# Optimization experiments

Measured on AMD Instinct MI355X. Metric: run time of the kernel, lower is better.

Reference implementation:

```python
import jax, jax.numpy as jnp
import numpy as np

B, S, DM = 1, 4096, 2048
H, HD = 16, 128
TS = 16          # tile_size
TOPK = 16        # anchor tiles per query
NUM_TILES = S // TS


def setup_inputs() -> dict:
    key = jax.random.key(0)
    ks = jax.random.split(key, 7)
    x = jax.random.normal(ks[0], (B, S, DM), jnp.float32)
    Wq = jax.random.normal(ks[1], (DM, H * HD), jnp.float32) * 0.02
    Wk = jax.random.normal(ks[2], (DM, H * HD), jnp.float32) * 0.02
    Wv = jax.random.normal(ks[3], (DM, H * HD), jnp.float32) * 0.02
    Wo = jax.random.normal(ks[4], (H * HD, DM), jnp.float32) * 0.02
    # RoPE angles: pos * inv_freq, shape [S, HD//2] (= freqs_cis angle)
    inv_freq = 1.0 / (10000.0 ** (np.arange(0, HD, 2, dtype=np.float32) / HD))
    freqs = jnp.asarray(np.arange(S, dtype=np.float32)[:, None] * inv_freq[None, :])
    anchor_indices = jax.random.randint(ks[5], (B, H, S, TOPK), 0, NUM_TILES).astype(jnp.int32)
    return {"x": x, "Wq": Wq, "Wk": Wk, "Wv": Wv, "Wo": Wo,
            "freqs": freqs, "anchor_indices": anchor_indices}


def _rotate_half(z):
    half = z.shape[-1] // 2
    return jnp.concatenate([-z[..., half:], z[..., :half]], axis=-1)


def reference(x, Wq, Wk, Wv, Wo, freqs, anchor_indices):
    b, s, _ = x.shape
    num_tiles = s // TS
    # QKV projections -> [B, H, S, HD]
    q = (x @ Wq).reshape(b, s, H, HD).transpose(0, 2, 1, 3)
    k = (x @ Wk).reshape(b, s, H, HD).transpose(0, 2, 1, 3)
    v = (x @ Wv).reshape(b, s, H, HD).transpose(0, 2, 1, 3)
    # RoPE (half-split / rotate_half convention), float32
    cos = jnp.cos(freqs)[None, None, :s, :]
    sin = jnp.sin(freqs)[None, None, :s, :]
    cos_full = jnp.concatenate([cos, cos], axis=-1)
    sin_full = jnp.concatenate([sin, sin], axis=-1)
    q = q * cos_full + _rotate_half(q) * sin_full
    k = k * cos_full + _rotate_half(k) * sin_full
    # Per-query tile indices: anchor tiles + local tile
    local_tiles = (jnp.arange(s) // TS).astype(jnp.int32)
    local = jnp.broadcast_to(local_tiles[None, None, :, None], (b, H, s, 1))
    tiles = jnp.concatenate([anchor_indices, local], axis=-1)  # [B,H,S,K+1]
    # Representative query per tile (last token of each query tile)
    tile_repr = jnp.arange(TS - 1, s, TS)
    tile_sel = tiles[:, :, tile_repr, :]                        # [B,H,T,K+1]
    # Expand tile indices to token indices
    offsets = jnp.arange(TS)
    token_idx = tile_sel[..., None] * TS + offsets              # [B,H,T,K+1,TS]
    sparse_len = tile_sel.shape[-1] * TS
    flat_idx = jnp.clip(token_idx.reshape(b, H, num_tiles, sparse_len), 0, s - 1)
    # Gather sparse K/V per (batch, head, query-tile)
    k_flat = k.reshape(b * H, s, HD)
    v_flat = v.reshape(b * H, s, HD)
    idx_flat = flat_idx.reshape(b * H, num_tiles, sparse_len)
    k_sparse = jax.vmap(lambda kv, idx: kv[idx])(k_flat, idx_flat)
    v_sparse = jax.vmap(lambda kv, idx: kv[idx])(v_flat, idx_flat)
    k_sparse = k_sparse.reshape(b, H, num_tiles, sparse_len, HD)
    v_sparse = v_sparse.reshape(b, H, num_tiles, sparse_len, HD)
    # Block-sparse attention per tile
    q_tiled = q.reshape(b, H, num_tiles, TS, HD)
    logits = jnp.einsum('bhtqd,bhtkd->bhtqk', q_tiled, k_sparse) / jnp.sqrt(HD)
    q_pos = jnp.arange(s).reshape(num_tiles, TS)
    future_mask = flat_idx[:, :, :, None, :] > q_pos[None, None, :, :, None]
    logits = jnp.where(future_mask, -1e10, logits)
    weights = jax.nn.softmax(logits, axis=-1)
    all_masked = jnp.all(future_mask, axis=-1, keepdims=True)
    weights = jnp.where(all_masked, 0.0, weights)
    weights = jnp.where(jnp.isnan(weights), 0.0, weights)
    out = jnp.einsum('bhtqk,bhtkd->bhtqd', weights, v_sparse)
    out = out.reshape(b, H, s, HD).transpose(0, 2, 1, 3).reshape(b, s, H * HD)
    return out @ Wo
```

## Files before the change

### kernel.cpp

```cpp
#include <hip/hip_runtime.h>

typedef unsigned short u16;
typedef unsigned int u32;
typedef __attribute__((ext_vector_type(8))) short bf16x8;
typedef __attribute__((ext_vector_type(4))) float f32x4;

__device__ __forceinline__ u16 f2bf(float f) {
  union { float f; u32 u; } v; v.f = f;
  u32 u = v.u;
  return (u16)((u + 0x7FFFu + ((u >> 16) & 1u)) >> 16);
}
__device__ __forceinline__ float bf2f(u16 s) {
  union { u32 u; float f; } v; v.u = ((u32)s) << 16;
  return v.f;
}

__device__ __forceinline__ void async16(const void* g, void* l) {
  __builtin_amdgcn_global_load_lds(
      (__attribute__((address_space(1))) void*)g,
      (__attribute__((address_space(3))) void*)l, 16, 0, 0);
}

__global__ void cast4_kernel(const float* __restrict__ in, u16* __restrict__ out, int n4) {
  int i = blockIdx.x * 256 + threadIdx.x;
  if (i < n4) {
    float4 v = ((const float4*)in)[i];
    ushort4 o;
    o.x = f2bf(v.x); o.y = f2bf(v.y); o.z = f2bf(v.z); o.w = f2bf(v.w);
    ((ushort4*)out)[i] = o;
  }
}

__global__ void transpose_cast_kernel(const float* __restrict__ in, u16* __restrict__ out,
                                      int R, int C) {
  __shared__ float tile[32][33];
  int c0 = blockIdx.x * 32, r0 = blockIdx.y * 32;
  int tx = threadIdx.x, ty = threadIdx.y;
#pragma unroll
  for (int i = ty; i < 32; i += 8) tile[i][tx] = in[(size_t)(r0 + i) * C + c0 + tx];
  __syncthreads();
#pragma unroll
  for (int i = ty; i < 32; i += 8)
    out[(size_t)(c0 + i) * R + r0 + tx] = f2bf(tile[tx][i]);
}

__global__ void trig_kernel(const float* __restrict__ freqs, float* __restrict__ ct,
                            float* __restrict__ st, int n) {
  int i = blockIdx.x * 256 + threadIdx.x;
  if (i < n) { float f = freqs[i]; ct[i] = cosf(f); st[i] = sinf(f); }
}

__global__ void rope_kernel(u16* __restrict__ q, u16* __restrict__ k,
                            const float* __restrict__ ct, const float* __restrict__ st) {
  int i = blockIdx.x * 256 + threadIdx.x;
  int dp = (i & 31) * 2;
  int hh = (i >> 5) & 15;
  int s  = i >> 9;
  float c0 = ct[s * 64 + dp], c1 = ct[s * 64 + dp + 1];
  float s0 = st[s * 64 + dp], s1 = st[s * 64 + dp + 1];
  size_t base = (size_t)s * 2048 + hh * 128 + dp;
  {
    u32 lo = *(u32*)(q + base);
    u32 hi = *(u32*)(q + base + 64);
    float a0 = bf2f((u16)lo), a1 = bf2f((u16)(lo >> 16));
    float b0 = bf2f((u16)hi), b1 = bf2f((u16)(hi >> 16));
    u32 nlo = (u32)f2bf(a0 * c0 - b0 * s0) | ((u32)f2bf(a1 * c1 - b1 * s1) << 16);
    u32 nhi = (u32)f2bf(b0 * c0 + a0 * s0) | ((u32)f2bf(b1 * c1 + a1 * s1) << 16);
    *(u32*)(q + base) = nlo;
    *(u32*)(q + base + 64) = nhi;
  }
  {
    u32 lo = *(u32*)(k + base);
    u32 hi = *(u32*)(k + base + 64);
    float a0 = bf2f((u16)lo), a1 = bf2f((u16)(lo >> 16));
    float b0 = bf2f((u16)hi), b1 = bf2f((u16)(hi >> 16));
    u32 nlo = (u32)f2bf(a0 * c0 - b0 * s0) | ((u32)f2bf(a1 * c1 - b1 * s1) << 16);
    u32 nhi = (u32)f2bf(b0 * c0 + a0 * s0) | ((u32)f2bf(b1 * c1 + a1 * s1) << 16);
    *(u32*)(k + base) = nlo;
    *(u32*)(k + base + 64) = nhi;
  }
}

__global__ void repack_k_kernel(const u16* __restrict__ Kin, u16* __restrict__ Kp) {
  const int h = blockIdx.y;
  const int s0 = blockIdx.x * 64;
  const int tid = threadIdx.x;
#pragma unroll
  for (int i = 0; i < 16; ++i) {
    int idx = i * 256 + tid;
    int r = idx >> 6;
    int d2 = idx & 63;
    u32 kv = ((const u32*)Kin)[(size_t)(s0 + r) * 1024 + h * 64 + d2];
    ((u32*)Kp)[((size_t)h * 4096 + s0 + r) * 64 + d2] = kv;
  }
}

__global__ void repack_v_kernel(const u16* __restrict__ Vin, u16* __restrict__ VT2) {
  const int h = blockIdx.y;
  const int s0 = blockIdx.x * 64;
  const int tid = threadIdx.x;
  __shared__ u16 lv[64][132];
#pragma unroll
  for (int i = 0; i < 16; ++i) {
    int idx = i * 256 + tid;
    int r = idx >> 6;
    int d2 = idx & 63;
    u32 vv = ((const u32*)Vin)[(size_t)(s0 + r) * 1024 + h * 64 + d2];
    *(u32*)(&lv[r][d2 * 2]) = vv;
  }
  __syncthreads();
#pragma unroll
  for (int i = 0; i < 16; ++i) {
    int idx = i * 256 + tid;
    int k2 = idx & 7;
    int d  = (idx >> 3) & 127;
    int tl = idx >> 10;
    u32 lo = lv[tl * 16 + k2 * 2][d];
    u32 hi = lv[tl * 16 + k2 * 2 + 1][d];
    ((u32*)VT2)[(((size_t)h * 256 + blockIdx.x * 4 + tl) * 128 + d) * 8 + k2] = lo | (hi << 16);
  }
}

template <int OUTBF>
__launch_bounds__(256, 2)
__global__ void gemm128_kernel(const u16* __restrict__ A, const u16* __restrict__ Bt,
                               void* __restrict__ C, int M, int N, int K) {
  __shared__ __align__(16) u16 As[128 * 64];
  __shared__ __align__(16) u16 Bs[128 * 64];
  const int tid  = threadIdx.x;
  const int lane = tid & 63;
  const int wave = tid >> 6;
  const int wr = wave >> 1, wc = wave & 1;
  const int brow = blockIdx.y * 128;
  const int bcol = blockIdx.x * 128;

  int a_goff[4], b_goff[4], l_off[4];
#pragma unroll
  for (int i = 0; i < 4; ++i) {
    int p = (wave * 4 + i) * 1024 + lane * 16;
    int row = p >> 7;
    int colb = (p & 127) ^ ((row & 7) << 4);
    a_goff[i] = (brow + row) * K + (colb >> 1);
    b_goff[i] = (bcol + row) * K + (colb >> 1);
    l_off[i] = p;
  }

  f32x4 acc[4][4];
#pragma unroll
  for (int m = 0; m < 4; ++m)
#pragma unroll
    for (int n = 0; n < 4; ++n) acc[m][n] = (f32x4){0.f, 0.f, 0.f, 0.f};

  for (int k0 = 0; k0 < K; k0 += 64) {
#pragma unroll
    for (int i = 0; i < 4; ++i) {
      async16(A + a_goff[i] + k0, (char*)As + l_off[i]);
      async16(Bt + b_goff[i] + k0, (char*)Bs + l_off[i]);
    }
    __syncthreads();
#pragma unroll
    for (int kk = 0; kk < 2; ++kk) {
      bf16x8 af[4], bfr[4];
#pragma unroll
      for (int m = 0; m < 4; ++m) {
        int row = wr * 64 + m * 16 + (lane & 15);
        int byte = (row << 7) + ((kk * 64 + ((lane >> 4) << 4)) ^ ((row & 7) << 4));
        af[m] = *(const bf16x8*)((const char*)As + byte);
      }
#pragma unroll
      for (int n = 0; n < 4; ++n) {
        int row = wc * 64 + n * 16 + (lane & 15);
        int byte = (row << 7) + ((kk * 64 + ((lane >> 4) << 4)) ^ ((row & 7) << 4));
        bfr[n] = *(const bf16x8*)((const char*)Bs + byte);
      }
#pragma unroll
      for (int m = 0; m < 4; ++m)
#pragma unroll
        for (int n = 0; n < 4; ++n)
          acc[m][n] = __builtin_amdgcn_mfma_f32_16x16x32_bf16(af[m], bfr[n], acc[m][n], 0, 0, 0);
    }
    __syncthreads();
  }

  const int r0 = brow + wr * 64;
  const int c0 = bcol + wc * 64;
#pragma unroll
  for (int m = 0; m < 4; ++m)
#pragma unroll
    for (int n = 0; n < 4; ++n)
#pragma unroll
      for (int r = 0; r < 4; ++r) {
        int rr = r0 + m * 16 + ((lane >> 4) << 2) + r;
        int cc = c0 + n * 16 + (lane & 15);
        if (OUTBF) ((u16*)C)[(size_t)rr * N + cc] = f2bf(acc[m][n][r]);
        else       ((float*)C)[(size_t)rr * N + cc] = acc[m][n][r];
      }
}

__launch_bounds__(256, 3)
__global__ void attn_kernel(const u16* __restrict__ Q, const u16* __restrict__ Kp,
                            const u16* __restrict__ VT2, const int* __restrict__ anchors,
                            u16* __restrict__ Out) {
  const int t = blockIdx.x;
  const int h = blockIdx.y;
  __shared__ int tiles[18];
  __shared__ float lg[16][292];
  __shared__ __align__(16) u16 w_lds[16][296];
  const int tid  = threadIdx.x;
  const int lane = tid & 63;
  const int wave = tid >> 6;
  const int g = lane >> 4;
  const int c = lane & 15;

  if (tid < 16) tiles[tid] = anchors[(size_t)((h << 12) + (t * 16 + 15)) * 16 + tid];
  if (tid == 16) tiles[16] = t;
  if (tid == 17) tiles[17] = 0;
  __syncthreads();

  {
    const u16* qbase = Q + (size_t)(t * 16 + c) * 2048 + h * 128 + g * 8;
    bf16x8 qf[4];
#pragma unroll
    for (int ks = 0; ks < 4; ++ks) qf[ks] = *(const bf16x8*)(qbase + ks * 32);
    for (int j = wave; j < 17; j += 4) {
      int tok = tiles[j] * 16 + c;
      const u16* kbase = Kp + ((size_t)h * 4096 + tok) * 128 + g * 8;
      f32x4 a = (f32x4){0.f, 0.f, 0.f, 0.f};
#pragma unroll
      for (int ks = 0; ks < 4; ++ks) {
        bf16x8 kf = *(const bf16x8*)(kbase + ks * 32);
        a = __builtin_amdgcn_mfma_f32_16x16x32_bf16(qf[ks], kf, a, 0, 0, 0);
      }
#pragma unroll
      for (int r = 0; r < 4; ++r) {
        int qrow = g * 4 + r;
        float vv = a[r] * 0.088388347648318447f;
        if (tok > t * 16 + qrow) vv = -1e10f;
        lg[qrow][j * 16 + c] = vv;
      }
    }
  }
  __syncthreads();

  {
    const int r = tid >> 4, cc = tid & 15;
    float vals[17];
    float mx = -3.0e38f;
#pragma unroll
    for (int i = 0; i < 17; ++i) { vals[i] = lg[r][i * 16 + cc]; mx = fmaxf(mx, vals[i]); }
#pragma unroll
    for (int d = 1; d < 16; d <<= 1) mx = fmaxf(mx, __shfl_xor(mx, d, 64));
    float sum = 0.f;
#pragma unroll
    for (int i = 0; i < 17; ++i) { vals[i] = __expf(vals[i] - mx); sum += vals[i]; }
#pragma unroll
    for (int d = 1; d < 16; d <<= 1) sum += __shfl_xor(sum, d, 64);
    float inv = sum > 0.f ? 1.0f / sum : 0.f;
#pragma unroll
    for (int i = 0; i < 17; ++i) w_lds[r][i * 16 + cc] = f2bf(vals[i] * inv);
    w_lds[r][272 + cc] = 0;
  }
  __syncthreads();

  {
    f32x4 o0 = (f32x4){0.f, 0.f, 0.f, 0.f}, o1 = o0;
    const int d0 = wave * 32;
    const size_t hb = (size_t)h * 256;
    const int keyin = (g & 1) * 8;
#pragma unroll
    for (int ks = 0; ks < 9; ++ks) {
      bf16x8 af = *(const bf16x8*)(&w_lds[c][ks * 32 + g * 8]);
      int jt = 2 * ks + (g >> 1);
      const u16* vb = VT2 + (hb + tiles[jt]) * 128 * 16;
      bf16x8 b0 = *(const bf16x8*)(vb + (d0 + c) * 16 + keyin);
      bf16x8 b1 = *(const bf16x8*)(vb + (d0 + 16 + c) * 16 + keyin);
      o0 = __builtin_amdgcn_mfma_f32_16x16x32_bf16(af, b0, o0, 0, 0, 0);
      o1 = __builtin_amdgcn_mfma_f32_16x16x32_bf16(af, b1, o1, 0, 0, 0);
    }
#pragma unroll
    for (int r = 0; r < 4; ++r) {
      int qrow = g * 4 + r;
      size_t base = (size_t)(t * 16 + qrow) * 2048 + h * 128;
      Out[base + d0 + c]      = f2bf(o0[r]);
      Out[base + d0 + 16 + c] = f2bf(o1[r]);
    }
  }
}

extern "C" void kernel_launch(void* const* d_in, const int* in_sizes, int n_in,
                              void* d_out, int out_size, void* d_ws, size_t ws_size,
                              hipStream_t stream) {
  (void)in_sizes; (void)n_in; (void)out_size; (void)ws_size;
  const float* x      = (const float*)d_in[0];
  const float* Wq     = (const float*)d_in[1];
  const float* Wk     = (const float*)d_in[2];
  const float* Wv     = (const float*)d_in[3];
  const float* Wo     = (const float*)d_in[4];
  const float* Wo_f   = (const float*)d_in[4];
  const float* freqs  = (const float*)d_in[5];
  const int* anchors  = (const int*)d_in[6];
  (void)Wo_f;
  float* out = (float*)d_out;

  char* ws = (char*)d_ws;
  const size_t MB = 1024 * 1024;
  u16* xbf   = (u16*)(ws + 0);
  u16* wqT   = (u16*)(ws + 16 * MB);
  u16* wkT   = (u16*)(ws + 24 * MB);
  u16* wvT   = (u16*)(ws + 32 * MB);
  u16* woT   = (u16*)(ws + 40 * MB);
  u16* qbf   = (u16*)(ws + 48 * MB);
  u16* kbf   = (u16*)(ws + 64 * MB);
  u16* vbf   = (u16*)(ws + 80 * MB);
  u16* attnb = (u16*)(ws + 0);
  u16* Kp    = (u16*)(ws + 16 * MB);
  float* ct  = (float*)(ws + 32 * MB);
  float* st  = (float*)(ws + 33 * MB);
  u16* VT2   = (u16*)(ws + 64 * MB);

  cast4_kernel<<<8192, 256, 0, stream>>>(x, xbf, 2097152);
  dim3 tb(32, 8), tg(64, 64);
  transpose_cast_kernel<<<tg, tb, 0, stream>>>(Wq, wqT, 2048, 2048);
  transpose_cast_kernel<<<tg, tb, 0, stream>>>(Wk, wkT, 2048, 2048);
  transpose_cast_kernel<<<tg, tb, 0, stream>>>(Wv, wvT, 2048, 2048);
  transpose_cast_kernel<<<tg, tb, 0, stream>>>(Wo, woT, 2048, 2048);

  dim3 gg(16, 32);
  gemm128_kernel<1><<<gg, 256, 0, stream>>>(xbf, wqT, qbf, 4096, 2048, 2048);
  gemm128_kernel<1><<<gg, 256, 0, stream>>>(xbf, wkT, kbf, 4096, 2048, 2048);
  gemm128_kernel<1><<<gg, 256, 0, stream>>>(xbf, wvT, vbf, 4096, 2048, 2048);
  trig_kernel<<<1024, 256, 0, stream>>>(freqs, ct, st, 262144);
  rope_kernel<<<8192, 256, 0, stream>>>(qbf, kbf, ct, st);
  repack_k_kernel<<<dim3(64, 16), 256, 0, stream>>>(kbf, Kp);
  repack_v_kernel<<<dim3(64, 16), 256, 0, stream>>>(vbf, VT2);
  attn_kernel<<<dim3(256, 16), 256, 0, stream>>>(qbf, Kp, VT2, anchors, attnb);
  gemm128_kernel<0><<<gg, 256, 0, stream>>>(attnb, woT, out, 4096, 2048, 2048);
}
```

Measured before the change: 280.7 us.

## Pipeline GEMMs with triple-buffered LDS and fuse K repack into RoPE

Replaces the 128x128 single-buffered GEMM with a 128x256-tile, 512-thread kernel. The new kernel triple-buffers LDS with async global-to-LDS loads, waits on vmcnt instead of a full barrier per tile, raises wave priority around the MFMA block and swizzles block order for L2 locality. Separately, RoPE now writes rotated K straight into the per-head packed layout, which drops the repack_k kernel and a pass over K. The attention kernel's occupancy hint goes from 3 to 5 blocks per CU, which may force register spills. The larger LDS footprint (about 144KB per block) limits GEMM occupancy.

Measured after the change: 309.7 us. 1.1x slower.

```diff
diff --git a/kernel.cpp b/kernel.cpp
--- a/kernel.cpp
+++ b/kernel.cpp
@@ -50,7 +50,8 @@
   if (i < n) { float f = freqs[i]; ct[i] = cosf(f); st[i] = sinf(f); }
 }
 
-__global__ void rope_kernel(u16* __restrict__ q, u16* __restrict__ k,
+__global__ void rope_kernel(u16* __restrict__ q, const u16* __restrict__ k,
+                            u16* __restrict__ Kp,
                             const float* __restrict__ ct, const float* __restrict__ st) {
   int i = blockIdx.x * 256 + threadIdx.x;
   int dp = (i & 31) * 2;
@@ -70,28 +71,15 @@
     *(u32*)(q + base + 64) = nhi;
   }
   {
-    u32 lo = *(u32*)(k + base);
-    u32 hi = *(u32*)(k + base + 64);
+    u32 lo = *(const u32*)(k + base);
+    u32 hi = *(const u32*)(k + base + 64);
     float a0 = bf2f((u16)lo), a1 = bf2f((u16)(lo >> 16));
     float b0 = bf2f((u16)hi), b1 = bf2f((u16)(hi >> 16));
     u32 nlo = (u32)f2bf(a0 * c0 - b0 * s0) | ((u32)f2bf(a1 * c1 - b1 * s1) << 16);
     u32 nhi = (u32)f2bf(b0 * c0 + a0 * s0) | ((u32)f2bf(b1 * c1 + a1 * s1) << 16);
-    *(u32*)(k + base) = nlo;
-    *(u32*)(k + base + 64) = nhi;
-  }
-}
-
-__global__ void repack_k_kernel(const u16* __restrict__ Kin, u16* __restrict__ Kp) {
-  const int h = blockIdx.y;
-  const int s0 = blockIdx.x * 64;
-  const int tid = threadIdx.x;
-#pragma unroll
-  for (int i = 0; i < 16; ++i) {
-    int idx = i * 256 + tid;
-    int r = idx >> 6;
-    int d2 = idx & 63;
-    u32 kv = ((const u32*)Kin)[(size_t)(s0 + r) * 1024 + h * 64 + d2];
-    ((u32*)Kp)[((size_t)h * 4096 + s0 + r) * 64 + d2] = kv;
+    size_t kpb = ((size_t)hh * 4096 + s) * 128 + dp;
+    *(u32*)(Kp + kpb) = nlo;
+    *(u32*)(Kp + kpb + 64) = nhi;
   }
 }
 
@@ -121,28 +109,73 @@
   }
 }
 
+__device__ __forceinline__ void tile_compute(const char* Asb, const char* Bsb,
+                                             int wm, int wn, int c, int g,
+                                             f32x4 (&acc)[4][4]) {
+  bf16x8 af[2][4], bb[2][4];
+  const int sw = (c & 7) << 4;
+#pragma unroll
+  for (int m = 0; m < 4; ++m) {
+    const int rb = (wm * 64 + m * 16 + c) << 7;
+#pragma unroll
+    for (int ks = 0; ks < 2; ++ks)
+      af[ks][m] = *(const bf16x8*)(Asb + rb + ((((ks * 4 + g) << 4) ^ sw)));
+  }
+#pragma unroll
+  for (int n = 0; n < 4; ++n) {
+    const int rb = (wn * 64 + n * 16 + c) << 7;
+#pragma unroll
+    for (int ks = 0; ks < 2; ++ks)
+      bb[ks][n] = *(const bf16x8*)(Bsb + rb + ((((ks * 4 + g) << 4) ^ sw)));
+  }
+  __builtin_amdgcn_s_setprio(1);
+#pragma unroll
+  for (int ks = 0; ks < 2; ++ks)
+#pragma unroll
+    for (int m = 0; m < 4; ++m)
+#pragma unroll
+      for (int n = 0; n < 4; ++n)
+        acc[m][n] = __builtin_amdgcn_mfma_f32_16x16x32_bf16(af[ks][m], bb[ks][n], acc[m][n], 0, 0, 0);
+  __builtin_amdgcn_s_setprio(0);
+}
+
 template <int OUTBF>
-__launch_bounds__(256, 2)
-__global__ void gemm128_kernel(const u16* __restrict__ A, const u16* __restrict__ Bt,
-                               void* __restrict__ C, int M, int N, int K) {
-  __shared__ __align__(16) u16 As[128 * 64];
-  __shared__ __align__(16) u16 Bs[128 * 64];
-  const int tid  = threadIdx.x;
+__launch_bounds__(512, 2)
+__global__ void gemm_pipe_kernel(const u16* __restrict__ A, const u16* __restrict__ Bt,
+                                 void* __restrict__ C, int M, int N, int K) {
+  __shared__ __align__(16) u16 As[3][128 * 64];
+  __shared__ __align__(16) u16 Bs[3][256 * 64];
+  const int tid = threadIdx.x;
   const int lane = tid & 63;
   const int wave = tid >> 6;
-  const int wr = wave >> 1, wc = wave & 1;
-  const int brow = blockIdx.y * 128;
-  const int bcol = blockIdx.x * 128;
-
-  int a_goff[4], b_goff[4], l_off[4];
-#pragma unroll
-  for (int i = 0; i < 4; ++i) {
-    int p = (wave * 4 + i) * 1024 + lane * 16;
+  const int wm = wave >> 2, wn = wave & 3;
+  const int c = lane & 15, g = lane >> 4;
+
+  const int nbx = gridDim.x, nby = gridDim.y;
+  const int nwg = nbx * nby;
+  const int bid = blockIdx.y * nbx + blockIdx.x;
+  const int sbid = (bid & 7) * (nwg >> 3) + (bid >> 3);
+  const int bx = sbid / nby;
+  const int by = sbid % nby;
+  const int brow = by * 128;
+  const int bcol = bx * 256;
+
+  int a_g[2], a_l[2], b_g[4], b_l[4];
+#pragma unroll
+  for (int i = 0; i < 2; ++i) {
+    int p = i * 8192 + tid * 16;
     int row = p >> 7;
     int colb = (p & 127) ^ ((row & 7) << 4);
-    a_goff[i] = (brow + row) * K + (colb >> 1);
-    b_goff[i] = (bcol + row) * K + (colb >> 1);
-    l_off[i] = p;
+    a_g[i] = (brow + row) * K + (colb >> 1);
+    a_l[i] = p;
+  }
+#pragma unroll
+  for (int i = 0; i < 4; ++i) {
+    int p = i * 8192 + tid * 16;
+    int row = p >> 7;
+    int colb = (p & 127) ^ ((row & 7) << 4);
+    b_g[i] = (bcol + row) * K + (colb >> 1);
+    b_l[i] = p;
   }
 
   f32x4 acc[4][4];
@@ -151,53 +184,47 @@
 #pragma unroll
     for (int n = 0; n < 4; ++n) acc[m][n] = (f32x4){0.f, 0.f, 0.f, 0.f};
 
-  for (int k0 = 0; k0 < K; k0 += 64) {
-#pragma unroll
-    for (int i = 0; i < 4; ++i) {
-      async16(A + a_goff[i] + k0, (char*)As + l_off[i]);
-      async16(Bt + b_goff[i] + k0, (char*)Bs + l_off[i]);
-    }
-    __syncthreads();
-#pragma unroll
-    for (int kk = 0; kk < 2; ++kk) {
-      bf16x8 af[4], bfr[4];
-#pragma unroll
-      for (int m = 0; m < 4; ++m) {
-        int row = wr * 64 + m * 16 + (lane & 15);
-        int byte = (row << 7) + ((kk * 64 + ((lane >> 4) << 4)) ^ ((row & 7) << 4));
-        af[m] = *(const bf16x8*)((const char*)As + byte);
-      }
-#pragma unroll
-      for (int n = 0; n < 4; ++n) {
-        int row = wc * 64 + n * 16 + (lane & 15);
-        int byte = (row << 7) + ((kk * 64 + ((lane >> 4) << 4)) ^ ((row & 7) << 4));
-        bfr[n] = *(const bf16x8*)((const char*)Bs + byte);
-      }
-#pragma unroll
-      for (int m = 0; m < 4; ++m)
-#pragma unroll
-        for (int n = 0; n < 4; ++n)
-          acc[m][n] = __builtin_amdgcn_mfma_f32_16x16x32_bf16(af[m], bfr[n], acc[m][n], 0, 0, 0);
-    }
-    __syncthreads();
-  }
-
-  const int r0 = brow + wr * 64;
-  const int c0 = bcol + wc * 64;
+  auto stage = [&](int bufi, int k0) {
+#pragma unroll
+    for (int i = 0; i < 2; ++i) async16(A + a_g[i] + k0, (char*)As[bufi] + a_l[i]);
+#pragma unroll
+    for (int i = 0; i < 4; ++i) async16(Bt + b_g[i] + k0, (char*)Bs[bufi] + b_l[i]);
+  };
+
+  const int nt = K >> 6;
+  stage(0, 0);
+  stage(1, 64);
+  int cur = 0, stg = 2;
+  for (int t = 0; t < nt - 1; ++t) {
+    asm volatile("s_waitcnt vmcnt(6)" ::: "memory");
+    __builtin_amdgcn_s_barrier();
+    __builtin_amdgcn_sched_barrier(0);
+    if (t + 2 < nt) stage(stg, (t + 2) << 6);
+    tile_compute((const char*)As[cur], (const char*)Bs[cur], wm, wn, c, g, acc);
+    cur = cur == 2 ? 0 : cur + 1;
+    stg = stg == 2 ? 0 : stg + 1;
+  }
+  asm volatile("s_waitcnt vmcnt(0)" ::: "memory");
+  __builtin_amdgcn_s_barrier();
+  __builtin_amdgcn_sched_barrier(0);
+  tile_compute((const char*)As[cur], (const char*)Bs[cur], wm, wn, c, g, acc);
+
+  const int r0 = brow + wm * 64;
+  const int c0 = bcol + wn * 64;
 #pragma unroll
   for (int m = 0; m < 4; ++m)
 #pragma unroll
     for (int n = 0; n < 4; ++n)
 #pragma unroll
       for (int r = 0; r < 4; ++r) {
-        int rr = r0 + m * 16 + ((lane >> 4) << 2) + r;
-        int cc = c0 + n * 16 + (lane & 15);
+        int rr = r0 + m * 16 + g * 4 + r;
+        int cc = c0 + n * 16 + c;
         if (OUTBF) ((u16*)C)[(size_t)rr * N + cc] = f2bf(acc[m][n][r]);
         else       ((float*)C)[(size_t)rr * N + cc] = acc[m][n][r];
       }
 }
 
-__launch_bounds__(256, 3)
+__launch_bounds__(256, 5)
 __global__ void attn_kernel(const u16* __restrict__ Q, const u16* __restrict__ Kp,
                             const u16* __restrict__ VT2, const int* __restrict__ anchors,
                             u16* __restrict__ Out) {
@@ -296,10 +323,8 @@
   const float* Wk     = (const float*)d_in[2];
   const float* Wv     = (const float*)d_in[3];
   const float* Wo     = (const float*)d_in[4];
-  const float* Wo_f   = (const float*)d_in[4];
   const float* freqs  = (const float*)d_in[5];
   const int* anchors  = (const int*)d_in[6];
-  (void)Wo_f;
   float* out = (float*)d_out;
 
   char* ws = (char*)d_ws;
@@ -325,14 +350,13 @@
   transpose_cast_kernel<<<tg, tb, 0, stream>>>(Wv, wvT, 2048, 2048);
   transpose_cast_kernel<<<tg, tb, 0, stream>>>(Wo, woT, 2048, 2048);
 
-  dim3 gg(16, 32);
-  gemm128_kernel<1><<<gg, 256, 0, stream>>>(xbf, wqT, qbf, 4096, 2048, 2048);
-  gemm128_kernel<1><<<gg, 256, 0, stream>>>(xbf, wkT, kbf, 4096, 2048, 2048);
-  gemm128_kernel<1><<<gg, 256, 0, stream>>>(xbf, wvT, vbf, 4096, 2048, 2048);
+  dim3 gp(8, 32);
+  gemm_pipe_kernel<1><<<gp, 512, 0, stream>>>(xbf, wqT, qbf, 4096, 2048, 2048);
+  gemm_pipe_kernel<1><<<gp, 512, 0, stream>>>(xbf, wkT, kbf, 4096, 2048, 2048);
+  gemm_pipe_kernel<1><<<gp, 512, 0, stream>>>(xbf, wvT, vbf, 4096, 2048, 2048);
   trig_kernel<<<1024, 256, 0, stream>>>(freqs, ct, st, 262144);
-  rope_kernel<<<8192, 256, 0, stream>>>(qbf, kbf, ct, st);
-  repack_k_kernel<<<dim3(64, 16), 256, 0, stream>>>(kbf, Kp);
+  rope_kernel<<<8192, 256, 0, stream>>>(qbf, kbf, Kp, ct, st);
   repack_v_kernel<<<dim3(64, 16), 256, 0, stream>>>(vbf, VT2);
   attn_kernel<<<dim3(256, 16), 256, 0, stream>>>(qbf, Kp, VT2, anchors, attnb);
-  gemm128_kernel<0><<<gg, 256, 0, stream>>>(attnb, woT, out, 4096, 2048, 2048);
-}
+  gemm_pipe_kernel<0><<<gp, 512, 0, stream>>>(attnb, woT, out, 4096, 2048, 2048);
+}
```
